# Performance work log

Measured on AMD Instinct MI355X. Metric: run time of the kernel, lower is better.

The kernel has to match this reference:

```python
import jax, jax.numpy as jnp
import numpy as np

GAMMA = 0.001

N_TEST, N_TRAIN, D, OUT = 8192, 8192, 512, 16

def setup_inputs() -> dict:
    key = jax.random.key(0)
    k1, k2, k3 = jax.random.split(key, 3)
    X = jax.random.normal(k1, (N_TEST, D), dtype=jnp.float32)
    train_X = jax.random.normal(k2, (N_TRAIN, D), dtype=jnp.float32)
    alpha = jax.random.normal(k3, (N_TRAIN, OUT), dtype=jnp.float32)
    return {"X": X, "train_X": train_X, "alpha": alpha}


def reference(X, train_X, alpha):
    # (same math as (x[:,None]-y[None])**2 summed over d, without the n*m*d blowup)
    x_sq = jnp.sum(X * X, axis=-1, keepdims=True)            # [n_test, 1]
    y_sq = jnp.sum(train_X * train_X, axis=-1)[None, :]       # [1, n_train]
    cross = X @ train_X.T                                     # [n_test, n_train]
    sq = x_sq + y_sq - 2.0 * cross
    K_test = jnp.exp(-GAMMA * sq)
    return K_test @ alpha                                     # [n_test, out]
```

## Files before the change

kernel.cpp:

```cpp
#include <hip/hip_runtime.h>
#include <stdint.h>

#define NROW 8192
#define DIM  512
#define NOUT 16
#define GAMMA 0.001f
#define EXP2S (2.0f * GAMMA * 1.44269504088896340736f)
#define SC1 0x7F7F7F7F

typedef __bf16 bf16_t;
typedef bf16_t bf16x4_t __attribute__((ext_vector_type(4)));
typedef bf16_t bf16x8_t __attribute__((ext_vector_type(8)));
typedef float  floatx4_t __attribute__((ext_vector_type(4)));
typedef int    intx4_t  __attribute__((ext_vector_type(4)));
typedef int    intx8_t  __attribute__((ext_vector_type(8)));

__device__ __forceinline__ void async_copy16(const void* g, const void* l) {
    __builtin_amdgcn_global_load_lds(
        (__attribute__((address_space(1))) void*)(uintptr_t)g,
        (__attribute__((address_space(3))) void*)(uint32_t)(uintptr_t)l,
        16, 0, 0);
}

__global__ __launch_bounds__(256) void prep_convert(
    const float* __restrict__ X, const float* __restrict__ T,
    const float* __restrict__ alpha,
    uint8_t* __restrict__ Xf, uint8_t* __restrict__ Tf,
    float* __restrict__ xfac, bf16_t* __restrict__ alphaTp)
{
    const int w = threadIdx.x >> 6, lane = threadIdx.x & 63;
    const int row = blockIdx.x * 4 + w;
    const bool is_test = row < NROW;
    const float* src = is_test ? X : T;
    uint8_t* dst = is_test ? Xf : Tf;
    const int r = is_test ? row : row - NROW;
    const float4* s4 = (const float4*)(src + (size_t)r * DIM);
    const float4 v0 = s4[lane * 2];
    const float4 v1 = s4[lane * 2 + 1];
    float ss = v0.x*v0.x + v0.y*v0.y + v0.z*v0.z + v0.w*v0.w
             + v1.x*v1.x + v1.y*v1.y + v1.z*v1.z + v1.w*v1.w;
    int lo = __builtin_amdgcn_cvt_pk_fp8_f32(v0.x, v0.y, 0, false);
    lo     = __builtin_amdgcn_cvt_pk_fp8_f32(v0.z, v0.w, lo, true);
    int hi = __builtin_amdgcn_cvt_pk_fp8_f32(v1.x, v1.y, 0, false);
    hi     = __builtin_amdgcn_cvt_pk_fp8_f32(v1.z, v1.w, hi, true);
    *(int2*)(dst + (size_t)r * DIM + lane * 8) = make_int2(lo, hi);
#pragma unroll
    for (int m = 32; m > 0; m >>= 1) ss += __shfl_xor(ss, m, 64);
    const float f = __expf(-GAMMA * ss);
    if (is_test) {
        if (lane == 0) xfac[r] = f;
    } else if (lane < 16) {
        alphaTp[(size_t)lane * NROW + r] = (bf16_t)(alpha[r * 16 + lane] * f);
    }
}

#define TPT 4
#define KLD2 72

__global__ __launch_bounds__(256, 2) void rbf_main(
    const uint8_t* __restrict__ Xf, const uint8_t* __restrict__ Tf,
    const bf16_t* __restrict__ alphaTp, const float* __restrict__ xfac,
    float* __restrict__ out)
{
    __shared__ __align__(16) unsigned char smem[65536];

    const int tid = threadIdx.x;
    const int w = tid >> 6, lane = tid & 63;
    const int wm = w >> 1, wn = w & 1;
    const int quad = lane >> 4, l15 = lane & 15;

    const int rb = blockIdx.x;
    const int chunk = blockIdx.y;
    const int row0 = rb * 128;
    const int cb0 = chunk * (TPT * 128);

    const int s_row = tid >> 3;
    const int s_ub = (((tid & 7) ^ (s_row & 7)) * 16);
    const uint8_t* gXp = Xf + (size_t)(row0 + s_row) * DIM + s_ub;
    const uint8_t* gTp = Tf + (size_t)(cb0 + s_row) * DIM + s_ub;
    const unsigned ldsW = (unsigned)(w << 10);

    const int sw = l15 & 7;

    const floatx4_t vzero = {0.f, 0.f, 0.f, 0.f};
    floatx4_t oacc[4];
#pragma unroll
    for (int i = 0; i < 4; ++i) oacc[i] = vzero;

    bf16_t* kw = (bf16_t*)smem + w * (64 * KLD2);

    for (int t = 0; t < TPT; ++t) {
        const int cb = cb0 + t * 128;
        const uint8_t* gTt = gTp + (size_t)t * 128 * DIM;

        floatx4_t acc[4][4];
#pragma unroll
        for (int i = 0; i < 4; ++i)
#pragma unroll
            for (int j = 0; j < 4; ++j) acc[i][j] = vzero;

        __syncthreads();
#pragma unroll
        for (int i = 0; i < 4; ++i) {
            async_copy16(gTt + (size_t)i * 16384, smem + i * 4096 + ldsW);
            async_copy16(gXp + (size_t)i * 16384, smem + 16384 + i * 4096 + ldsW);
        }

#pragma unroll
        for (int g = 0; g < 4; ++g) {
            __syncthreads();
            if (g < 3) {
                const unsigned bb = ((g + 1) & 1) * 32768u;
                const int kb = (g + 1) * 128;
#pragma unroll
                for (int i = 0; i < 4; ++i) {
                    async_copy16(gTt + (size_t)i * 16384 + kb, smem + bb + i * 4096 + ldsW);
                    async_copy16(gXp + (size_t)i * 16384 + kb, smem + bb + 16384 + i * 4096 + ldsW);
                }
            }
            const unsigned char* bufc = smem + (g & 1) * 32768;
            intx8_t ta[4], xb[4];
#pragma unroll
            for (int i = 0; i < 4; ++i) {
                const int rA = wm * 64 + i * 16 + l15;
                const intx4_t alo = *(const intx4_t*)(bufc + rA * 128 + (((2 * quad) ^ sw) * 16));
                const intx4_t ahi = *(const intx4_t*)(bufc + rA * 128 + (((2 * quad + 1) ^ sw) * 16));
                ta[i] = __builtin_shufflevector(alo, ahi, 0, 1, 2, 3, 4, 5, 6, 7);
                const int rB = wn * 64 + i * 16 + l15;
                const intx4_t blo = *(const intx4_t*)(bufc + 16384 + rB * 128 + (((2 * quad) ^ sw) * 16));
                const intx4_t bhi = *(const intx4_t*)(bufc + 16384 + rB * 128 + (((2 * quad + 1) ^ sw) * 16));
                xb[i] = __builtin_shufflevector(blo, bhi, 0, 1, 2, 3, 4, 5, 6, 7);
            }
#pragma unroll
            for (int mi = 0; mi < 4; ++mi)
#pragma unroll
                for (int ni = 0; ni < 4; ++ni)
                    acc[mi][ni] = __builtin_amdgcn_mfma_scale_f32_16x16x128_f8f6f4(
                        ta[mi], xb[ni], acc[mi][ni], 0, 0, 0, SC1, 0, SC1);
        }

        __syncthreads();
#pragma unroll
        for (int ni = 0; ni < 4; ++ni)
#pragma unroll
            for (int mi = 0; mi < 4; ++mi) {
                bf16x4_t pk;
#pragma unroll
                for (int r = 0; r < 4; ++r)
                    pk[r] = (bf16_t)__builtin_amdgcn_exp2f(acc[mi][ni][r] * EXP2S);
                *(bf16x4_t*)(kw + (ni * 16 + l15) * KLD2 + mi * 16 + quad * 4) = pk;
            }

#pragma unroll
        for (int ks = 0; ks < 2; ++ks) {
            const bf16x8_t bv = *(const bf16x8_t*)(alphaTp + (size_t)l15 * NROW
                                                   + cb + wm * 64 + ks * 32 + quad * 8);
#pragma unroll
            for (int ni = 0; ni < 4; ++ni) {
                const bf16x8_t av = *(const bf16x8_t*)(kw + (ni * 16 + l15) * KLD2
                                                       + ks * 32 + quad * 8);
                oacc[ni] = __builtin_amdgcn_mfma_f32_16x16x32_bf16(av, bv, oacc[ni], 0, 0, 0);
            }
        }
    }

    __syncthreads();
    float* stash = (float*)smem;
    if (wm == 1) {
#pragma unroll
        for (int ni = 0; ni < 4; ++ni)
            *(floatx4_t*)(stash + wn * 1024 + ni * 256 + lane * 4) = oacc[ni];
    }
    __syncthreads();
    if (wm == 0) {
#pragma unroll
        for (int ni = 0; ni < 4; ++ni) {
            const floatx4_t o2 = *(const floatx4_t*)(stash + wn * 1024 + ni * 256 + lane * 4);
            const int trow = row0 + wn * 64 + ni * 16 + quad * 4;
            const float4 xf = *(const float4*)(xfac + trow);
            atomicAdd(out + (size_t)(trow + 0) * NOUT + l15, (oacc[ni][0] + o2[0]) * xf.x);
            atomicAdd(out + (size_t)(trow + 1) * NOUT + l15, (oacc[ni][1] + o2[1]) * xf.y);
            atomicAdd(out + (size_t)(trow + 2) * NOUT + l15, (oacc[ni][2] + o2[2]) * xf.z);
            atomicAdd(out + (size_t)(trow + 3) * NOUT + l15, (oacc[ni][3] + o2[3]) * xf.w);
        }
    }
}

extern "C" void kernel_launch(void* const* d_in, const int* in_sizes, int n_in,
                              void* d_out, int out_size, void* d_ws, size_t ws_size,
                              hipStream_t stream) {
    (void)in_sizes; (void)n_in; (void)out_size; (void)ws_size;
    const float* X     = (const float*)d_in[0];
    const float* T     = (const float*)d_in[1];
    const float* alpha = (const float*)d_in[2];

    char* ws = (char*)d_ws;
    uint8_t* Xf     = (uint8_t*)ws;
    uint8_t* Tf     = (uint8_t*)(ws + (8u << 20));
    float*   xfac   = (float*)(ws + (16u << 20));
    bf16_t*  alphaTp= (bf16_t*)(ws + (16u << 20) + (64u << 10));
    float*   out    = (float*)d_out;

    hipMemsetAsync(out, 0, (size_t)NROW * NOUT * sizeof(float), stream);
    prep_convert<<<4096, 256, 0, stream>>>(X, T, alpha, Xf, Tf, xfac, alphaTp);
    dim3 grid(64, 16);
    rbf_main<<<grid, 256, 0, stream>>>(Xf, Tf, alphaTp, xfac, out);
}
```

Baseline: 121.6 us.

## Keep test-row FP8 operand tiles resident in registers across train tiles

Each wave now loads its 64 test rows of the FP8 X operand (all 512 dims) from global memory into registers once, instead of staging them through LDS for every one of the four train tiles. Only the train tile is double-buffered in LDS, so the shared buffer shrinks to 36 KB and LDS traffic and async copies per tile are halved. The trade-off is 128 extra VGPRs per thread, which under launch_bounds(256,2) risks spilling or lower occupancy.

After: 136.7 us. 12.4% more time.

```diff
diff --git a/kernel.cpp b/kernel.cpp
--- a/kernel.cpp
+++ b/kernel.cpp
@@ -62,7 +62,7 @@
     const bf16_t* __restrict__ alphaTp, const float* __restrict__ xfac,
     float* __restrict__ out)
 {
-    __shared__ __align__(16) unsigned char smem[65536];
+    __shared__ __align__(16) unsigned char smem[36864];
 
     const int tid = threadIdx.x;
     const int w = tid >> 6, lane = tid & 63;
@@ -76,12 +76,20 @@
 
     const int s_row = tid >> 3;
     const int s_ub = (((tid & 7) ^ (s_row & 7)) * 16);
-    const uint8_t* gXp = Xf + (size_t)(row0 + s_row) * DIM + s_ub;
     const uint8_t* gTp = Tf + (size_t)(cb0 + s_row) * DIM + s_ub;
     const unsigned ldsW = (unsigned)(w << 10);
 
     const int sw = l15 & 7;
 
+    intx8_t xg[4][4];
+#pragma unroll
+    for (int g = 0; g < 4; ++g)
+#pragma unroll
+        for (int i = 0; i < 4; ++i)
+            xg[g][i] = *(const intx8_t*)(Xf
+                + (size_t)(row0 + wn * 64 + i * 16 + l15) * DIM
+                + g * 128 + quad * 32);
+
     const floatx4_t vzero = {0.f, 0.f, 0.f, 0.f};
     floatx4_t oacc[4];
 #pragma unroll
@@ -90,8 +98,7 @@
     bf16_t* kw = (bf16_t*)smem + w * (64 * KLD2);
 
     for (int t = 0; t < TPT; ++t) {
-        const int cb = cb0 + t * 128;
-        const uint8_t* gTt = gTp + (size_t)t * 128 * DIM;
+        const uint8_t* gTt = gTp + (size_t)(cb0 ? 0 : 0) + (size_t)t * 128 * DIM;
 
         floatx4_t acc[4][4];
 #pragma unroll
@@ -101,42 +108,31 @@
 
         __syncthreads();
 #pragma unroll
-        for (int i = 0; i < 4; ++i) {
+        for (int i = 0; i < 4; ++i)
             async_copy16(gTt + (size_t)i * 16384, smem + i * 4096 + ldsW);
-            async_copy16(gXp + (size_t)i * 16384, smem + 16384 + i * 4096 + ldsW);
-        }
 
 #pragma unroll
         for (int g = 0; g < 4; ++g) {
             __syncthreads();
             if (g < 3) {
-                const unsigned bb = ((g + 1) & 1) * 32768u;
+                const unsigned bb = ((g + 1) & 1) * 16384u;
                 const int kb = (g + 1) * 128;
 #pragma unroll
-                for (int i = 0; i < 4; ++i) {
+                for (int i = 0; i < 4; ++i)
                     async_copy16(gTt + (size_t)i * 16384 + kb, smem + bb + i * 4096 + ldsW);
-                    async_copy16(gXp + (size_t)i * 16384 + kb, smem + bb + 16384 + i * 4096 + ldsW);
-                }
-            }
-            const unsigned char* bufc = smem + (g & 1) * 32768;
-            intx8_t ta[4], xb[4];
-#pragma unroll
-            for (int i = 0; i < 4; ++i) {
-                const int rA = wm * 64 + i * 16 + l15;
+            }
+            const unsigned char* bufc = smem + (g & 1) * 16384;
+#pragma unroll
+            for (int mi = 0; mi < 4; ++mi) {
+                const int rA = wm * 64 + mi * 16 + l15;
                 const intx4_t alo = *(const intx4_t*)(bufc + rA * 128 + (((2 * quad) ^ sw) * 16));
                 const intx4_t ahi = *(const intx4_t*)(bufc + rA * 128 + (((2 * quad + 1) ^ sw) * 16));
-                ta[i] = __builtin_shufflevector(alo, ahi, 0, 1, 2, 3, 4, 5, 6, 7);
-                const int rB = wn * 64 + i * 16 + l15;
-                const intx4_t blo = *(const intx4_t*)(bufc + 16384 + rB * 128 + (((2 * quad) ^ sw) * 16));
-                const intx4_t bhi = *(const intx4_t*)(bufc + 16384 + rB * 128 + (((2 * quad + 1) ^ sw) * 16));
-                xb[i] = __builtin_shufflevector(blo, bhi, 0, 1, 2, 3, 4, 5, 6, 7);
-            }
-#pragma unroll
-            for (int mi = 0; mi < 4; ++mi)
+                const intx8_t ta = __builtin_shufflevector(alo, ahi, 0, 1, 2, 3, 4, 5, 6, 7);
 #pragma unroll
                 for (int ni = 0; ni < 4; ++ni)
                     acc[mi][ni] = __builtin_amdgcn_mfma_scale_f32_16x16x128_f8f6f4(
-                        ta[mi], xb[ni], acc[mi][ni], 0, 0, 0, SC1, 0, SC1);
+                        ta, xg[g][ni], acc[mi][ni], 0, 0, 0, SC1, 0, SC1);
+            }
         }
 
         __syncthreads();
@@ -151,6 +147,7 @@
                 *(bf16x4_t*)(kw + (ni * 16 + l15) * KLD2 + mi * 16 + quad * 4) = pk;
             }
 
+        const int cb = cb0 + t * 128;
 #pragma unroll
         for (int ks = 0; ks < 2; ++ks) {
             const bf16x8_t bv = *(const bf16x8_t*)(alphaTp + (size_t)l15 * NROW
```
